# Kernel optimization log

Hardware: AMD Instinct MI355X
Metric: run time of the kernel (lower is better)

Reference implementation:

```python
import jax, jax.numpy as jnp
import numpy as np

E = 1024
H = 16
DH = E // H
EPS = 1e-8
GRAM_W = 1.5


def _gram_scores(q, k1, k2):
    # q: [BH, L, D], k1/k2: [BH, S, D] -> [BH, L, S]
    ll = jnp.sum(q * q, -1)[:, :, None]          # [BH, L, 1]
    vv = jnp.sum(k1 * k1, -1)[:, None, :]        # [BH, 1, S]
    aa = jnp.sum(k2 * k2, -1)[:, None, :]
    va = jnp.sum(k1 * k2, -1)[:, None, :]
    lv = jnp.einsum('bld,bsd->bls', q, k1)
    la = jnp.einsum('bld,bsd->bls', q, k2)
    det = ll * (vv * aa - va * va) - lv * (lv * aa - la * va) + la * (lv * va - la * vv)
    return -jnp.sqrt(jnp.clip(det, EPS, None))


def setup_inputs() -> dict:
    key = jax.random.key(0)
    ks = jax.random.split(key, 20)
    L, B, S = 512, 4, 1024
    inp = {
        'query': jax.random.normal(ks[0], (L, B, E), jnp.float32),
        'mod1': jax.random.normal(ks[1], (S, B, E), jnp.float32),
        'mod2': jax.random.normal(ks[2], (S, B, E), jnp.float32),
    }
    # Linear params stored as [in, out] (y = x @ W + b), 8 linears
    names = ['q', 'k1', 'k2', 'v1', 'v2', 'g1', 'g2', 'o']
    for i, n in enumerate(names):
        inp[n + '_w'] = jax.random.normal(ks[3 + 2 * i], (E, E), jnp.float32) * 0.02
        inp[n + '_b'] = jax.random.normal(ks[4 + 2 * i], (E,), jnp.float32) * 0.02
    return inp


def reference(query, mod1, mod2,
              q_w, q_b, k1_w, k1_b, k2_w, k2_b, v1_w, v1_b, v2_w, v2_b,
              g1_w, g1_b, g2_w, g2_b, o_w, o_b):
    L, B, _ = query.shape
    S = mod1.shape[0]
    scaling = DH ** -0.5

    def lin(x, w, b):
        return x @ w + b

    def split_heads(x, n):  # [n, B, E] -> [B*H, n, DH]
        return x.reshape(n, B * H, DH).transpose(1, 0, 2)

    q = split_heads(lin(query, q_w, q_b) * scaling, L)
    k1 = split_heads(lin(mod1, k1_w, k1_b), S)
    k2 = split_heads(lin(mod2, k2_w, k2_b), S)
    v1 = split_heads(lin(mod1, v1_w, v1_b), S)
    v2 = split_heads(lin(mod2, v2_w, v2_b), S)

    w1 = jnp.einsum('bld,bsd->bls', q, k1)
    w2 = jnp.einsum('bld,bsd->bls', q, k2)
    gram = _gram_scores(q, k1, k2)
    logits = GRAM_W * gram + w1 + w2          # [BH, L, S]
    attn = jax.nn.softmax(logits, axis=-1)

    def merge_heads(x):  # [B*H, L, DH] -> [L, B, E]
        return x.transpose(1, 0, 2).reshape(L, B, E)

    out1 = merge_heads(jnp.einsum('bls,bsd->bld', attn, v1))
    out2 = merge_heads(jnp.einsum('bls,bsd->bld', attn, v2))
    gate1 = jax.nn.sigmoid(lin(query, g1_w, g1_b))
    gate2 = jax.nn.sigmoid(lin(query, g2_w, g2_b))
    attn_output = lin((out1 * gate1 + out2 * gate2) / 2.0, o_w, o_b)
    avg_weights = attn.reshape(B, H, L, S).mean(axis=1)
    return attn_output, avg_weights
```

## Files before the change

kernel.cpp:

```cpp
#include <hip/hip_runtime.h>
#include <cstddef>
#include <cstdint>

typedef unsigned short ushort_t;
typedef unsigned int uint_t;
typedef __attribute__((ext_vector_type(8))) short short8;
typedef __attribute__((ext_vector_type(4))) float f32x4;

#define EDIM 1024
#define NHEAD 16
#define HDIM 64
#define NB 4
#define LQ 512
#define SK 1024
#define BHD 64

__device__ __forceinline__ ushort_t f2b(float f) {
    uint_t u = __float_as_uint(f);
    return (ushort_t)((u + 0x7fffu + ((u >> 16) & 1u)) >> 16);
}
__device__ __forceinline__ float b2f(ushort_t b) {
    return __uint_as_float(((uint_t)b) << 16);
}

__device__ __forceinline__ void gload_lds16(const void* g, void* l) {
    __builtin_amdgcn_global_load_lds((const __attribute__((address_space(1))) void*)g,
                                     (__attribute__((address_space(3))) void*)l, 16, 0, 0);
}

template<int OUTMODE>
__global__ __launch_bounds__(256, 2)
void gemm_mfma(const ushort_t* __restrict__ Ah, const ushort_t* __restrict__ Al,
               const ushort_t* __restrict__ Bh, const ushort_t* __restrict__ Bl,
               const float* __restrict__ b0, const float* __restrict__ b1,
               const float* __restrict__ b2,
               void* __restrict__ Y0, void* __restrict__ Y1, void* __restrict__ Y2,
               float scale)
{
    __shared__ ushort_t As[128 * 64];
    __shared__ ushort_t Bs[128 * 64];
    const int tid = threadIdx.x;
    const int wave = tid >> 6, lane = tid & 63;
    const int ln = lane & 15, lq = lane >> 4;
    const int row0 = blockIdx.y * 128, col0 = blockIdx.x * 128;
    const int wm = wave & 1, wn = wave >> 1;
    const int cswz = (lane & 7) ^ ((lane >> 3) & 7);
    const int mrl = lane >> 3;

    const int seg = (OUTMODE == 0) ? 0 : (blockIdx.x >> 3);
    const int NPASS = (OUTMODE == 5 && seg == 0) ? 3 : 1;

    f32x4 zero = {0.f, 0.f, 0.f, 0.f};
    f32x4 acc[4][4];
#pragma unroll
    for (int i = 0; i < 4; ++i)
#pragma unroll
        for (int j = 0; j < 4; ++j) acc[i][j] = zero;

    for (int pp = 0; pp < NPASS; ++pp) {
        const ushort_t* Ab = (pp == 2) ? Al : Ah;
        const ushort_t* Bb = (pp == 1) ? Bl : Bh;
        for (int kk = 0; kk < 1024; kk += 64) {
            __syncthreads();
#pragma unroll
            for (int j = 0; j < 4; ++j) {
                const int mr = (wave * 4 + j) * 8 + mrl;
                gload_lds16(Ab + (size_t)(row0 + mr) * 1024 + kk + cswz * 8,
                            (void*)(As + (wave * 4 + j) * 512));
                gload_lds16(Bb + (size_t)(col0 + mr) * 1024 + kk + cswz * 8,
                            (void*)(Bs + (wave * 4 + j) * 512));
            }
            __syncthreads();
#pragma unroll
            for (int sub = 0; sub < 2; ++sub) {
                short8 af[4], bfv[4];
#pragma unroll
                for (int i = 0; i < 4; ++i) {
                    const int ml = wm * 64 + i * 16 + ln;
                    af[i] = *(const short8*)(As + ml * 64 + (((sub * 4 + lq) ^ (ml & 7)) * 8));
                    const int nl = wn * 64 + i * 16 + ln;
                    bfv[i] = *(const short8*)(Bs + nl * 64 + (((sub * 4 + lq) ^ (nl & 7)) * 8));
                }
#pragma unroll
                for (int i = 0; i < 4; ++i)
#pragma unroll
                    for (int j = 0; j < 4; ++j)
                        acc[i][j] = __builtin_amdgcn_mfma_f32_16x16x32_bf16(af[i], bfv[j], acc[i][j], 0, 0, 0);
            }
        }
    }

    const float* bias = (seg == 0) ? b0 : ((seg == 1) ? b1 : b2);

#pragma unroll
    for (int i = 0; i < 4; ++i) {
#pragma unroll
        for (int r = 0; r < 4; ++r) {
            const int row = row0 + wm * 64 + i * 16 + lq * 4 + r;
#pragma unroll
            for (int j = 0; j < 4; ++j) {
                const int col = col0 + wn * 64 + j * 16 + ln;
                const int lc = col & 1023;
                float v = acc[i][j][r] + bias[lc];
                if (OUTMODE == 0) {
                    ((float*)Y0)[(size_t)row * 1024 + lc] = v;
                } else if (OUTMODE == 4) {
                    if (seg == 0) {
                        v *= scale;
                        const int s = row >> 2, b = row & 3, h = lc >> 6, d = lc & 63;
                        ((ushort_t*)Y0)[(((size_t)(b * 16 + h)) * 512 + s) * 64 + d] = f2b(v);
                    } else {
                        v = 1.0f / (1.0f + __expf(-v));
                        float* Y = (seg == 1) ? (float*)Y1 : (float*)Y2;
                        Y[(size_t)row * 1024 + lc] = v;
                    }
                } else {
                    const int s = row >> 2, b = row & 3, h = lc >> 6, d = lc & 63;
                    const size_t addr = (((size_t)(b * 16 + h)) * 1024 + s) * 64 + d;
                    if (seg == 0) ((float*)Y0)[addr] = v;
                    else          ((ushort_t*)Y1)[addr] = f2b(v);
                }
            }
        }
    }
}

__global__ __launch_bounds__(256)
void cast_q_kernel(const float* __restrict__ x, ushort_t* __restrict__ y)
{
    const size_t i = ((size_t)blockIdx.x * 256 + threadIdx.x) * 8;
    float4 a = *(const float4*)(x + i);
    float4 b = *(const float4*)(x + i + 4);
    ushort_t o[8] = {f2b(a.x), f2b(a.y), f2b(a.z), f2b(a.w), f2b(b.x), f2b(b.y), f2b(b.z), f2b(b.w)};
    *(uint4*)( (void*)(y + i) ) = *(const uint4*)o;
}

__global__ __launch_bounds__(256)
void cast_mod_kernel(const float* __restrict__ m1, const float* __restrict__ m2,
                     ushort_t* __restrict__ h1, ushort_t* __restrict__ l1,
                     ushort_t* __restrict__ h2, ushort_t* __restrict__ l2)
{
    const float* x = blockIdx.y ? m2 : m1;
    ushort_t* yh = blockIdx.y ? h2 : h1;
    ushort_t* yl = blockIdx.y ? l2 : l1;
    const size_t i = ((size_t)blockIdx.x * 256 + threadIdx.x) * 8;
    float v[8];
    *(float4*)v = *(const float4*)(x + i);
    *(float4*)(v + 4) = *(const float4*)(x + i + 4);
    ushort_t oh[8], ol[8];
#pragma unroll
    for (int k = 0; k < 8; ++k) {
        oh[k] = f2b(v[k]);
        ol[k] = f2b(v[k] - b2f(oh[k]));
    }
    *(uint4*)( (void*)(yh + i) ) = *(const uint4*)oh;
    *(uint4*)( (void*)(yl + i) ) = *(const uint4*)ol;
}

struct WArgs {
    const float* src[8];
    ushort_t* hi[8];
    ushort_t* lo[8];
};
__global__ __launch_bounds__(256)
void wcast_kernel(WArgs args)
{
    __shared__ float T[64][65];
    const int z = blockIdx.z;
    const float* W = args.src[z];
    ushort_t* Th = args.hi[z];
    ushort_t* Tl = args.lo[z];
    const int k0 = blockIdx.x * 64, n0 = blockIdx.y * 64;
    const int tid = threadIdx.x;
    const int r = tid >> 2, cg = (tid & 3) * 16;
#pragma unroll
    for (int u = 0; u < 4; ++u) {
        float4 v = *(const float4*)(W + (size_t)(k0 + r) * 1024 + n0 + cg + u * 4);
        T[r][cg + u * 4 + 0] = v.x; T[r][cg + u * 4 + 1] = v.y;
        T[r][cg + u * 4 + 2] = v.z; T[r][cg + u * 4 + 3] = v.w;
    }
    __syncthreads();
    ushort_t oh[16], ol[16];
#pragma unroll
    for (int u = 0; u < 16; ++u) {
        float v = T[cg + u][r];
        oh[u] = f2b(v);
        ol[u] = f2b(v - b2f(oh[u]));
    }
    ushort_t* dh = Th + (size_t)(n0 + r) * 1024 + k0 + cg;
    *(uint4*)( (void*)dh ) = *(const uint4*)oh;
    *(uint4*)( (void*)(dh + 8) ) = *(const uint4*)(oh + 8);
    if (Tl) {
        ushort_t* dl = Tl + (size_t)(n0 + r) * 1024 + k0 + cg;
        *(uint4*)( (void*)dl ) = *(const uint4*)ol;
        *(uint4*)( (void*)(dl + 8) ) = *(const uint4*)(ol + 8);
    }
}

__global__ __launch_bounds__(256)
void norms_cast_k_kernel(const float* __restrict__ K1f, const float* __restrict__ K2f,
                         ushort_t* __restrict__ K1b, ushort_t* __restrict__ K2b,
                         float* __restrict__ vv, float* __restrict__ aa, float* __restrict__ va)
{
    const int wave = threadIdx.x >> 6, lane = threadIdx.x & 63;
    const int row = blockIdx.x * 4 + wave;
    const float x1 = K1f[(size_t)row * 64 + lane];
    const float x2 = K2f[(size_t)row * 64 + lane];
    K1b[(size_t)row * 64 + lane] = f2b(x1);
    K2b[(size_t)row * 64 + lane] = f2b(x2);
    float s1 = x1 * x1, s2 = x2 * x2, s3 = x1 * x2;
#pragma unroll
    for (int o = 1; o < 64; o <<= 1) {
        s1 += __shfl_xor(s1, o);
        s2 += __shfl_xor(s2, o);
        s3 += __shfl_xor(s3, o);
    }
    if (lane == 0) { vv[row] = s1; aa[row] = s2; va[row] = s3; }
}

__global__ __launch_bounds__(256)
void normsq_kernel(const ushort_t* __restrict__ Qb, float* __restrict__ ll)
{
    const int wave = threadIdx.x >> 6, lane = threadIdx.x & 63;
    const int row = blockIdx.x * 4 + wave;
    const float x = b2f(Qb[(size_t)row * 64 + lane]);
    float s = x * x;
#pragma unroll
    for (int o = 1; o < 64; o <<= 1) s += __shfl_xor(s, o);
    if (lane == 0) ll[row] = s;
}

__global__ __launch_bounds__(256)
void vtrans_kernel(const ushort_t* __restrict__ V1b, const ushort_t* __restrict__ V2b,
                   ushort_t* __restrict__ V1t, ushort_t* __restrict__ V2t)
{
    __shared__ float T[64][65];
    const ushort_t* S = blockIdx.z ? V2b : V1b;
    ushort_t* D = blockIdx.z ? V2t : V1t;
    const int bh = blockIdx.y, s0 = blockIdx.x * 64;
    const int tid = threadIdx.x;
    const int r = tid >> 2, cg = (tid & 3) * 16;
    ushort_t buf[16];
    const ushort_t* sp = S + ((size_t)bh * 1024 + s0 + r) * 64 + cg;
    *(uint4*)buf = *(const uint4*)sp;
    *(uint4*)(buf + 8) = *(const uint4*)(sp + 8);
#pragma unroll
    for (int u = 0; u < 16; ++u) T[r][cg + u] = b2f(buf[u]);
    __syncthreads();
    ushort_t o[16];
#pragma unroll
    for (int u = 0; u < 16; ++u) o[u] = f2b(T[cg + u][r]);
    ushort_t* d = D + ((size_t)bh * 64 + r) * 1024 + s0 + cg;
    *(uint4*)( (void*)d ) = *(const uint4*)o;
    *(uint4*)( (void*)(d + 8) ) = *(const uint4*)(o + 8);
}

__global__ __launch_bounds__(256, 2)
void scores_kernel(const ushort_t* __restrict__ Qb, const ushort_t* __restrict__ K1b,
                   const ushort_t* __restrict__ K2b, const float* __restrict__ ll,
                   const float* __restrict__ vv, const float* __restrict__ aa,
                   const float* __restrict__ va, float* __restrict__ logits)
{
    __shared__ ushort_t Qs[128 * 64];
    __shared__ ushort_t K1s[128 * 64];
    __shared__ ushort_t K2s[128 * 64];
    __shared__ float llS[128], vvS[128], aaS[128], vaS[128];
    const int tid = threadIdx.x;
    const int wave = tid >> 6, lane = tid & 63;
    const int ln = lane & 15, lq = lane >> 4;
    const int wm = wave & 1, wn = wave >> 1;
    const int bh = blockIdx.z;
    const int l0 = blockIdx.y * 128, s0 = blockIdx.x * 128;
    const int cswz = (lane & 7) ^ ((lane >> 3) & 7);
    const int mrl = lane >> 3;

    if (tid < 128) {
        llS[tid] = ll[(size_t)bh * 512 + l0 + tid];
        vvS[tid] = vv[(size_t)bh * 1024 + s0 + tid];
        aaS[tid] = aa[(size_t)bh * 1024 + s0 + tid];
        vaS[tid] = va[(size_t)bh * 1024 + s0 + tid];
    }
#pragma unroll
    for (int j = 0; j < 4; ++j) {
        const int mr = (wave * 4 + j) * 8 + mrl;
        gload_lds16(Qb + ((size_t)bh * 512 + l0 + mr) * 64 + cswz * 8, (void*)(Qs + (wave * 4 + j) * 512));
        gload_lds16(K1b + ((size_t)bh * 1024 + s0 + mr) * 64 + cswz * 8, (void*)(K1s + (wave * 4 + j) * 512));
        gload_lds16(K2b + ((size_t)bh * 1024 + s0 + mr) * 64 + cswz * 8, (void*)(K2s + (wave * 4 + j) * 512));
    }
    __syncthreads();

    f32x4 zero = {0.f, 0.f, 0.f, 0.f};
    f32x4 lv[4][4], la[4][4];
#pragma unroll
    for (int i = 0; i < 4; ++i)
#pragma unroll
        for (int j = 0; j < 4; ++j) { lv[i][j] = zero; la[i][j] = zero; }

#pragma unroll
    for (int sub = 0; sub < 2; ++sub) {
        short8 qf[4], k1f[4], k2f[4];
#pragma unroll
        for (int i = 0; i < 4; ++i) {
            const int ml = wm * 64 + i * 16 + ln;
            qf[i] = *(const short8*)(Qs + ml * 64 + (((sub * 4 + lq) ^ (ml & 7)) * 8));
            const int nl = wn * 64 + i * 16 + ln;
            k1f[i] = *(const short8*)(K1s + nl * 64 + (((sub * 4 + lq) ^ (nl & 7)) * 8));
            k2f[i] = *(const short8*)(K2s + nl * 64 + (((sub * 4 + lq) ^ (nl & 7)) * 8));
        }
#pragma unroll
        for (int i = 0; i < 4; ++i)
#pragma unroll
            for (int j = 0; j < 4; ++j) {
                lv[i][j] = __builtin_amdgcn_mfma_f32_16x16x32_bf16(qf[i], k1f[j], lv[i][j], 0, 0, 0);
                la[i][j] = __builtin_amdgcn_mfma_f32_16x16x32_bf16(qf[i], k2f[j], la[i][j], 0, 0, 0);
            }
    }

#pragma unroll
    for (int i = 0; i < 4; ++i) {
#pragma unroll
        for (int r = 0; r < 4; ++r) {
            const int l_loc = wm * 64 + i * 16 + lq * 4 + r;
            const float LL = llS[l_loc];
#pragma unroll
            for (int j = 0; j < 4; ++j) {
                const int s_loc = wn * 64 + j * 16 + ln;
                const float VV = vvS[s_loc], AA = aaS[s_loc], VA = vaS[s_loc];
                const float LV = lv[i][j][r], LA = la[i][j][r];
                float det = LL * (VV * AA - VA * VA) - LV * (LV * AA - LA * VA) + LA * (LV * VA - LA * VV);
                det = fmaxf(det, 1e-8f);
                logits[((size_t)bh * 512 + l0 + l_loc) * 1024 + s0 + s_loc] = LV + LA - 1.5f * sqrtf(det);
            }
        }
    }
}

__global__ __launch_bounds__(256)
void softmax_avg_kernel(float* __restrict__ logits, float* __restrict__ avg)
{
    __shared__ float part[4][1024];
    const int b = blockIdx.x >> 9, l = blockIdx.x & 511;
    const int wave = threadIdx.x >> 6, lane = threadIdx.x & 63;
    float pacc[16];
#pragma unroll
    for (int u = 0; u < 16; ++u) pacc[u] = 0.f;
#pragma unroll
    for (int jj = 0; jj < 4; ++jj) {
        const int h = wave * 4 + jj;
        float* rowp = logits + (((size_t)(b * 16 + h)) * 512 + l) * 1024;
        float4 v[4];
#pragma unroll
        for (int c = 0; c < 4; ++c) v[c] = *(const float4*)(rowp + c * 256 + lane * 4);
        float m = -3.4e38f;
#pragma unroll
        for (int c = 0; c < 4; ++c) m = fmaxf(m, fmaxf(fmaxf(v[c].x, v[c].y), fmaxf(v[c].z, v[c].w)));
#pragma unroll
        for (int o = 1; o < 64; o <<= 1) m = fmaxf(m, __shfl_xor(m, o));
        float s = 0.f;
#pragma unroll
        for (int c = 0; c < 4; ++c) {
            v[c].x = __expf(v[c].x - m); v[c].y = __expf(v[c].y - m);
            v[c].z = __expf(v[c].z - m); v[c].w = __expf(v[c].w - m);
            s += v[c].x + v[c].y + v[c].z + v[c].w;
        }
#pragma unroll
        for (int o = 1; o < 64; o <<= 1) s += __shfl_xor(s, o);
        const float inv = 1.0f / s;
        ushort_t* arow = (ushort_t*)rowp;
#pragma unroll
        for (int c = 0; c < 4; ++c) {
            const float p0 = v[c].x * inv, p1 = v[c].y * inv, p2 = v[c].z * inv, p3 = v[c].w * inv;
            ushort_t w[4] = {f2b(p0), f2b(p1), f2b(p2), f2b(p3)};
            *(uint2*)( (void*)(arow + c * 256 + lane * 4) ) = *(const uint2*)w;
            pacc[c * 4 + 0] += p0; pacc[c * 4 + 1] += p1;
            pacc[c * 4 + 2] += p2; pacc[c * 4 + 3] += p3;
        }
    }
#pragma unroll
    for (int c = 0; c < 4; ++c) {
        float4 pv = {pacc[c * 4 + 0], pacc[c * 4 + 1], pacc[c * 4 + 2], pacc[c * 4 + 3]};
        *(float4*)(&part[wave][c * 256 + lane * 4]) = pv;
    }
    __syncthreads();
    const int s0 = threadIdx.x * 4;
    float4 a0 = *(const float4*)(&part[0][s0]);
    float4 a1 = *(const float4*)(&part[1][s0]);
    float4 a2 = *(const float4*)(&part[2][s0]);
    float4 a3 = *(const float4*)(&part[3][s0]);
    float4 o;
    o.x = (a0.x + a1.x + a2.x + a3.x) * 0.0625f;
    o.y = (a0.y + a1.y + a2.y + a3.y) * 0.0625f;
    o.z = (a0.z + a1.z + a2.z + a3.z) * 0.0625f;
    o.w = (a0.w + a1.w + a2.w + a3.w) * 0.0625f;
    *(float4*)(avg + ((size_t)(b * 512 + l)) * 1024 + s0) = o;
}

__global__ __launch_bounds__(256, 2)
void pv_gate_kernel(const ushort_t* __restrict__ attn, const ushort_t* __restrict__ V1t,
                    const ushort_t* __restrict__ V2t, const float* __restrict__ G1,
                    const float* __restrict__ G2, ushort_t* __restrict__ tmpb)
{
    __shared__ ushort_t Ps[128 * 64];
    __shared__ ushort_t V1s[64 * 64];
    __shared__ ushort_t V2s[64 * 64];
    const int tid = threadIdx.x;
    const int wave = tid >> 6, lane = tid & 63;
    const int ln = lane & 15, lq = lane >> 4;
    const int bh = blockIdx.y;
    const int l0 = blockIdx.x * 128;
    const int cswz = (lane & 7) ^ ((lane >> 3) & 7);
    const int mrl = lane >> 3;
    const int bq = bh >> 4, h = bh & 15;

    f32x4 zero = {0.f, 0.f, 0.f, 0.f};
    f32x4 acc1[2][4], acc2[2][4];
#pragma unroll
    for (int i = 0; i < 2; ++i)
#pragma unroll
        for (int j = 0; j < 4; ++j) { acc1[i][j] = zero; acc2[i][j] = zero; }

    for (int s0 = 0; s0 < 1024; s0 += 64) {
        __syncthreads();
#pragma unroll
        for (int j = 0; j < 4; ++j) {
            const int mr = (wave * 4 + j) * 8 + mrl;
            gload_lds16(attn + ((size_t)bh * 512 + l0 + mr) * 2048 + s0 + cswz * 8,
                        (void*)(Ps + (wave * 4 + j) * 512));
        }
#pragma unroll
        for (int j = 0; j < 2; ++j) {
            const int mv = (wave * 2 + j) * 8 + mrl;
            gload_lds16(V1t + ((size_t)bh * 64 + mv) * 1024 + s0 + cswz * 8,
                        (void*)(V1s + (wave * 2 + j) * 512));
            gload_lds16(V2t + ((size_t)bh * 64 + mv) * 1024 + s0 + cswz * 8,
                        (void*)(V2s + (wave * 2 + j) * 512));
        }
        __syncthreads();
#pragma unroll
        for (int sub = 0; sub < 2; ++sub) {
            short8 af[2], b1f[4], b2f_[4];
#pragma unroll
            for (int i = 0; i < 2; ++i) {
                const int ml = wave * 32 + i * 16 + ln;
                af[i] = *(const short8*)(Ps + ml * 64 + (((sub * 4 + lq) ^ (ml & 7)) * 8));
            }
#pragma unroll
            for (int j = 0; j < 4; ++j) {
                const int nl = j * 16 + ln;
                b1f[j] = *(const short8*)(V1s + nl * 64 + (((sub * 4 + lq) ^ (nl & 7)) * 8));
                b2f_[j] = *(const short8*)(V2s + nl * 64 + (((sub * 4 + lq) ^ (nl & 7)) * 8));
            }
#pragma unroll
            for (int i = 0; i < 2; ++i)
#pragma unroll
                for (int j = 0; j < 4; ++j) {
                    acc1[i][j] = __builtin_amdgcn_mfma_f32_16x16x32_bf16(af[i], b1f[j], acc1[i][j], 0, 0, 0);
                    acc2[i][j] = __builtin_amdgcn_mfma_f32_16x16x32_bf16(af[i], b2f_[j], acc2[i][j], 0, 0, 0);
                }
        }
    }

#pragma unroll
    for (int i = 0; i < 2; ++i) {
#pragma unroll
        for (int r = 0; r < 4; ++r) {
            const int l = l0 + wave * 32 + i * 16 + lq * 4 + r;
#pragma unroll
            for (int j = 0; j < 4; ++j) {
                const int d = j * 16 + ln;
                const size_t addr = ((size_t)l * 4 + bq) * 1024 + h * 64 + d;
                const float v = 0.5f * (acc1[i][j][r] * G1[addr] + acc2[i][j][r] * G2[addr]);
                tmpb[addr] = f2b(v);
            }
        }
    }
}

extern "C" void kernel_launch(void* const* d_in, const int* in_sizes, int n_in,
                              void* d_out, int out_size, void* d_ws, size_t ws_size,
                              hipStream_t stream)
{
    const float* query = (const float*)d_in[0];
    const float* mod1  = (const float*)d_in[1];
    const float* mod2  = (const float*)d_in[2];
    const float* q_w  = (const float*)d_in[3];  const float* q_b  = (const float*)d_in[4];
    const float* k1_w = (const float*)d_in[5];  const float* k1_b = (const float*)d_in[6];
    const float* k2_w = (const float*)d_in[7];  const float* k2_b = (const float*)d_in[8];
    const float* v1_w = (const float*)d_in[9];  const float* v1_b = (const float*)d_in[10];
    const float* v2_w = (const float*)d_in[11]; const float* v2_b = (const float*)d_in[12];
    const float* g1_w = (const float*)d_in[13]; const float* g1_b = (const float*)d_in[14];
    const float* g2_w = (const float*)d_in[15]; const float* g2_b = (const float*)d_in[16];
    const float* o_w  = (const float*)d_in[17]; const float* o_b  = (const float*)d_in[18];
    float* out = (float*)d_out;

    const size_t MB = 1u << 20;
    char* w = (char*)d_ws;
    ushort_t* Wqg  = (ushort_t*)(w + 0 * MB);
    ushort_t* Wkv1 = (ushort_t*)(w + 6 * MB);
    ushort_t* Wkv2 = (ushort_t*)(w + 10 * MB);
    ushort_t* Wo   = (ushort_t*)(w + 14 * MB);
    ushort_t* Wk1l = (ushort_t*)(w + 16 * MB);
    ushort_t* Wk2l = (ushort_t*)(w + 18 * MB);
    ushort_t* qx   = (ushort_t*)(w + 20 * MB);
    ushort_t* tmpb = qx;
    ushort_t* m1h  = (ushort_t*)(w + 24 * MB);
    ushort_t* m2h  = (ushort_t*)(w + 32 * MB);
    float* G1 = (float*)(w + 24 * MB);
    float* G2 = (float*)(w + 32 * MB);
    ushort_t* Qb  = (ushort_t*)(w + 40 * MB);
    ushort_t* K1b = (ushort_t*)(w + 44 * MB);
    ushort_t* K2b = (ushort_t*)(w + 52 * MB);
    ushort_t* V1t = (ushort_t*)(w + 60 * MB);
    ushort_t* V2t = (ushort_t*)(w + 68 * MB);
    float* ll = (float*)(w + 76 * MB);
    float* vv = (float*)(w + 76 * MB + 256 * 1024);
    float* aa = (float*)(w + 76 * MB + 512 * 1024);
    float* va = (float*)(w + 76 * MB + 768 * 1024);
    float* logits = (float*)(w + 78 * MB);
    float* K1f = (float*)(w + 78 * MB);
    float* K2f = (float*)(w + 94 * MB);
    ushort_t* V1b = (ushort_t*)(w + 110 * MB);
    ushort_t* V2b = (ushort_t*)(w + 118 * MB);
    ushort_t* m1l = (ushort_t*)(w + 190 * MB);
    ushort_t* m2l = (ushort_t*)(w + 198 * MB);
    ushort_t* attn = (ushort_t*)logits;

    cast_q_kernel<<<1024, 256, 0, stream>>>(query, qx);
    cast_mod_kernel<<<dim3(2048, 2), 256, 0, stream>>>(mod1, mod2, m1h, m1l, m2h, m2l);
    WArgs wa;
    const float* srcs[8] = {q_w, g1_w, g2_w, k1_w, v1_w, k2_w, v2_w, o_w};
    ushort_t* his[8] = {Wqg, Wqg + (size_t)1024 * 1024, Wqg + (size_t)2048 * 1024,
                        Wkv1, Wkv1 + (size_t)1024 * 1024, Wkv2, Wkv2 + (size_t)1024 * 1024, Wo};
    ushort_t* los[8] = {nullptr, nullptr, nullptr, Wk1l, nullptr, Wk2l, nullptr, nullptr};
    for (int i = 0; i < 8; ++i) { wa.src[i] = srcs[i]; wa.hi[i] = his[i]; wa.lo[i] = los[i]; }
    wcast_kernel<<<dim3(16, 16, 8), 256, 0, stream>>>(wa);

    gemm_mfma<5><<<dim3(16, 32), 256, 0, stream>>>(m1h, m1l, Wkv1, Wk1l, k1_b, v1_b, nullptr,
                                                   K1f, V1b, nullptr, 1.f);
    gemm_mfma<5><<<dim3(16, 32), 256, 0, stream>>>(m2h, m2l, Wkv2, Wk2l, k2_b, v2_b, nullptr,
                                                   K2f, V2b, nullptr, 1.f);
    gemm_mfma<4><<<dim3(24, 16), 256, 0, stream>>>(qx, nullptr, Wqg, nullptr, q_b, g1_b, g2_b,
                                                   Qb, G1, G2, 0.125f);

    norms_cast_k_kernel<<<16384, 256, 0, stream>>>(K1f, K2f, K1b, K2b, vv, aa, va);
    normsq_kernel<<<8192, 256, 0, stream>>>(Qb, ll);
    vtrans_kernel<<<dim3(16, 64, 2), 256, 0, stream>>>(V1b, V2b, V1t, V2t);

    scores_kernel<<<dim3(8, 4, 64), 256, 0, stream>>>(Qb, K1b, K2b, ll, vv, aa, va, logits);
    softmax_avg_kernel<<<2048, 256, 0, stream>>>(logits, out + (size_t)LQ * NB * EDIM);
    pv_gate_kernel<<<dim3(4, 64), 256, 0, stream>>>(attn, V1t, V2t, G1, G2, tmpb);

    gemm_mfma<0><<<dim3(8, 16), 256, 0, stream>>>(tmpb, nullptr, Wo, nullptr, o_b, nullptr, nullptr,
                                                  out, nullptr, nullptr, 1.f);
}
```

Baseline: 436.1 us.

## Merge projection GEMMs, cast and prep kernels into fewer launches

Combines the three cast kernels into one launch and the three input-projection GEMMs into a single grid. In that grid the 3-pass split-precision K blocks are separated from the 1-pass V blocks, so per-block work is more uniform. The norm, norm-squared and V-transpose kernels are merged into one prep launch, gates are stored as bf16 instead of fp32, and the output projection uses 64-row tiles to put more blocks on the device. The intent is to cut launch gaps and tail effects and to reduce gate memory traffic, at the cost of bf16 rounding on the gate values.

```diff
diff --git a/kernel.cpp b/kernel.cpp
--- a/kernel.cpp
+++ b/kernel.cpp
@@ -28,27 +28,51 @@
                                      (__attribute__((address_space(3))) void*)l, 16, 0, 0);
 }
 
-template<int OUTMODE>
+struct MegaArgs {
+    const ushort_t *qx, *m1h, *m1l, *m2h, *m2l;
+    const ushort_t *Wqg, *Wkv1, *Wkv2, *Wk1l, *Wk2l;
+    const float *q_b, *k1_b, *k2_b, *v1_b, *v2_b, *g1_b, *g2_b;
+    float *K1f, *K2f;
+    ushort_t *V1b, *V2b, *Qb, *G1b, *G2b;
+};
+
 __global__ __launch_bounds__(256, 2)
-void gemm_mfma(const ushort_t* __restrict__ Ah, const ushort_t* __restrict__ Al,
-               const ushort_t* __restrict__ Bh, const ushort_t* __restrict__ Bl,
-               const float* __restrict__ b0, const float* __restrict__ b1,
-               const float* __restrict__ b2,
-               void* __restrict__ Y0, void* __restrict__ Y1, void* __restrict__ Y2,
-               float scale)
+void mega_gemm(MegaArgs a)
 {
     __shared__ ushort_t As[128 * 64];
     __shared__ ushort_t Bs[128 * 64];
     const int tid = threadIdx.x;
     const int wave = tid >> 6, lane = tid & 63;
     const int ln = lane & 15, lq = lane >> 4;
-    const int row0 = blockIdx.y * 128, col0 = blockIdx.x * 128;
     const int wm = wave & 1, wn = wave >> 1;
     const int cswz = (lane & 7) ^ ((lane >> 3) & 7);
     const int mrl = lane >> 3;
 
-    const int seg = (OUTMODE == 0) ? 0 : (blockIdx.x >> 3);
-    const int NPASS = (OUTMODE == 5 && seg == 0) ? 3 : 1;
+    const int id = blockIdx.x;
+    const ushort_t *A, *Al, *B, *Bl;
+    const float* bias;
+    int npass, row0, col0, kind;
+    if (id < 512) {
+        kind = id >> 8;
+        const int t = id & 255;
+        col0 = (t & 7) * 128; row0 = (t >> 3) * 128; npass = 3;
+        A = kind ? a.m2h : a.m1h;  Al = kind ? a.m2l : a.m1l;
+        B = kind ? a.Wkv2 : a.Wkv1; Bl = kind ? a.Wk2l : a.Wk1l;
+        bias = kind ? a.k2_b : a.k1_b;
+    } else if (id < 1024) {
+        int t = id - 512; kind = 2 + (t >> 8); t &= 255;
+        col0 = (t & 7) * 128; row0 = (t >> 3) * 128; npass = 1;
+        A = (kind == 2) ? a.m1h : a.m2h; Al = A;
+        B = ((kind == 2) ? a.Wkv1 : a.Wkv2) + (size_t)1024 * 1024; Bl = B;
+        bias = (kind == 2) ? a.v1_b : a.v2_b;
+    } else {
+        const int t = id - 1024; kind = 4;
+        const int c = t % 24, rr = t / 24;
+        col0 = c * 128; row0 = rr * 128; npass = 1;
+        A = a.qx; Al = A; B = a.Wqg; Bl = B;
+        const int seg = c >> 3;
+        bias = (seg == 0) ? a.q_b : ((seg == 1) ? a.g1_b : a.g2_b);
+    }
 
     f32x4 zero = {0.f, 0.f, 0.f, 0.f};
     f32x4 acc[4][4];
@@ -57,9 +81,9 @@
 #pragma unroll
         for (int j = 0; j < 4; ++j) acc[i][j] = zero;
 
-    for (int pp = 0; pp < NPASS; ++pp) {
-        const ushort_t* Ab = (pp == 2) ? Al : Ah;
-        const ushort_t* Bb = (pp == 1) ? Bl : Bh;
+    for (int pp = 0; pp < npass; ++pp) {
+        const ushort_t* Ab = (pp == 2) ? Al : A;
+        const ushort_t* Bb = (pp == 1) ? Bl : B;
         for (int kk = 0; kk < 1024; kk += 64) {
             __syncthreads();
 #pragma unroll
@@ -90,8 +114,6 @@
         }
     }
 
-    const float* bias = (seg == 0) ? b0 : ((seg == 1) ? b1 : b2);
-
 #pragma unroll
     for (int i = 0; i < 4; ++i) {
 #pragma unroll
@@ -102,157 +124,155 @@
                 const int col = col0 + wn * 64 + j * 16 + ln;
                 const int lc = col & 1023;
                 float v = acc[i][j][r] + bias[lc];
-                if (OUTMODE == 0) {
-                    ((float*)Y0)[(size_t)row * 1024 + lc] = v;
-                } else if (OUTMODE == 4) {
+                if (kind <= 1) {
+                    const int s = row >> 2, b = row & 3, h = lc >> 6, d = lc & 63;
+                    float* Y = kind ? a.K2f : a.K1f;
+                    Y[(((size_t)(b * 16 + h)) * 1024 + s) * 64 + d] = v;
+                } else if (kind <= 3) {
+                    const int s = row >> 2, b = row & 3, h = lc >> 6, d = lc & 63;
+                    ushort_t* Y = (kind == 2) ? a.V1b : a.V2b;
+                    Y[(((size_t)(b * 16 + h)) * 1024 + s) * 64 + d] = f2b(v);
+                } else {
+                    const int seg = col >> 10;
                     if (seg == 0) {
-                        v *= scale;
+                        v *= 0.125f;
                         const int s = row >> 2, b = row & 3, h = lc >> 6, d = lc & 63;
-                        ((ushort_t*)Y0)[(((size_t)(b * 16 + h)) * 512 + s) * 64 + d] = f2b(v);
+                        a.Qb[(((size_t)(b * 16 + h)) * 512 + s) * 64 + d] = f2b(v);
                     } else {
                         v = 1.0f / (1.0f + __expf(-v));
-                        float* Y = (seg == 1) ? (float*)Y1 : (float*)Y2;
-                        Y[(size_t)row * 1024 + lc] = v;
+                        ushort_t* Y = (seg == 1) ? a.G1b : a.G2b;
+                        Y[(size_t)row * 1024 + lc] = f2b(v);
                     }
-                } else {
-                    const int s = row >> 2, b = row & 3, h = lc >> 6, d = lc & 63;
-                    const size_t addr = (((size_t)(b * 16 + h)) * 1024 + s) * 64 + d;
-                    if (seg == 0) ((float*)Y0)[addr] = v;
-                    else          ((ushort_t*)Y1)[addr] = f2b(v);
                 }
             }
         }
     }
 }
 
+struct CastArgs {
+    const float* q; const float* m1; const float* m2;
+    ushort_t* qx; ushort_t* m1h; ushort_t* m1l; ushort_t* m2h; ushort_t* m2l;
+    const float* wsrc[8];
+    ushort_t* whi[8];
+    ushort_t* wlo[8];
+};
+
 __global__ __launch_bounds__(256)
-void cast_q_kernel(const float* __restrict__ x, ushort_t* __restrict__ y)
-{
-    const size_t i = ((size_t)blockIdx.x * 256 + threadIdx.x) * 8;
-    float4 a = *(const float4*)(x + i);
-    float4 b = *(const float4*)(x + i + 4);
-    ushort_t o[8] = {f2b(a.x), f2b(a.y), f2b(a.z), f2b(a.w), f2b(b.x), f2b(b.y), f2b(b.z), f2b(b.w)};
-    *(uint4*)( (void*)(y + i) ) = *(const uint4*)o;
+void casts_kernel(CastArgs a)
+{
+    __shared__ float T[64][65];
+    const int id = blockIdx.x;
+    const int tid = threadIdx.x;
+    if (id < 1024) {
+        const size_t i = ((size_t)id * 256 + tid) * 8;
+        float4 x = *(const float4*)(a.q + i);
+        float4 y = *(const float4*)(a.q + i + 4);
+        ushort_t o[8] = {f2b(x.x), f2b(x.y), f2b(x.z), f2b(x.w), f2b(y.x), f2b(y.y), f2b(y.z), f2b(y.w)};
+        *(uint4*)( (void*)(a.qx + i) ) = *(const uint4*)o;
+    } else if (id < 5120) {
+        const int t = id - 1024;
+        const int which = t >> 11;
+        const float* x = which ? a.m2 : a.m1;
+        ushort_t* yh = which ? a.m2h : a.m1h;
+        ushort_t* yl = which ? a.m2l : a.m1l;
+        const size_t i = ((size_t)(t & 2047) * 256 + tid) * 8;
+        float v[8];
+        *(float4*)v = *(const float4*)(x + i);
+        *(float4*)(v + 4) = *(const float4*)(x + i + 4);
+        ushort_t oh[8], ol[8];
+#pragma unroll
+        for (int k = 0; k < 8; ++k) {
+            oh[k] = f2b(v[k]);
+            ol[k] = f2b(v[k] - b2f(oh[k]));
+        }
+        *(uint4*)( (void*)(yh + i) ) = *(const uint4*)oh;
+        *(uint4*)( (void*)(yl + i) ) = *(const uint4*)ol;
+    } else {
+        const int t = id - 5120;
+        const int z = t >> 8, x = t & 15, y = (t >> 4) & 15;
+        const float* W = a.wsrc[z];
+        ushort_t* Th = a.whi[z];
+        ushort_t* Tl = a.wlo[z];
+        const int k0 = x * 64, n0 = y * 64;
+        const int r = tid >> 2, cg = (tid & 3) * 16;
+#pragma unroll
+        for (int u = 0; u < 4; ++u) {
+            float4 v = *(const float4*)(W + (size_t)(k0 + r) * 1024 + n0 + cg + u * 4);
+            T[r][cg + u * 4 + 0] = v.x; T[r][cg + u * 4 + 1] = v.y;
+            T[r][cg + u * 4 + 2] = v.z; T[r][cg + u * 4 + 3] = v.w;
+        }
+        __syncthreads();
+        ushort_t oh[16], ol[16];
+#pragma unroll
+        for (int u = 0; u < 16; ++u) {
+            float v = T[cg + u][r];
+            oh[u] = f2b(v);
+            ol[u] = f2b(v - b2f(oh[u]));
+        }
+        ushort_t* dh = Th + (size_t)(n0 + r) * 1024 + k0 + cg;
+        *(uint4*)( (void*)dh ) = *(const uint4*)oh;
+        *(uint4*)( (void*)(dh + 8) ) = *(const uint4*)(oh + 8);
+        if (Tl) {
+            ushort_t* dl = Tl + (size_t)(n0 + r) * 1024 + k0 + cg;
+            *(uint4*)( (void*)dl ) = *(const uint4*)ol;
+            *(uint4*)( (void*)(dl + 8) ) = *(const uint4*)(ol + 8);
+        }
+    }
 }
 
 __global__ __launch_bounds__(256)
-void cast_mod_kernel(const float* __restrict__ m1, const float* __restrict__ m2,
-                     ushort_t* __restrict__ h1, ushort_t* __restrict__ l1,
-                     ushort_t* __restrict__ h2, ushort_t* __restrict__ l2)
-{
-    const float* x = blockIdx.y ? m2 : m1;
-    ushort_t* yh = blockIdx.y ? h2 : h1;
-    ushort_t* yl = blockIdx.y ? l2 : l1;
-    const size_t i = ((size_t)blockIdx.x * 256 + threadIdx.x) * 8;
-    float v[8];
-    *(float4*)v = *(const float4*)(x + i);
-    *(float4*)(v + 4) = *(const float4*)(x + i + 4);
-    ushort_t oh[8], ol[8];
-#pragma unroll
-    for (int k = 0; k < 8; ++k) {
-        oh[k] = f2b(v[k]);
-        ol[k] = f2b(v[k] - b2f(oh[k]));
-    }
-    *(uint4*)( (void*)(yh + i) ) = *(const uint4*)oh;
-    *(uint4*)( (void*)(yl + i) ) = *(const uint4*)ol;
-}
-
-struct WArgs {
-    const float* src[8];
-    ushort_t* hi[8];
-    ushort_t* lo[8];
-};
-__global__ __launch_bounds__(256)
-void wcast_kernel(WArgs args)
+void prep_kernel(const float* __restrict__ K1f, const float* __restrict__ K2f,
+                 ushort_t* __restrict__ K1b, ushort_t* __restrict__ K2b,
+                 float* __restrict__ vv, float* __restrict__ aa, float* __restrict__ va,
+                 const ushort_t* __restrict__ Qb, float* __restrict__ ll,
+                 const ushort_t* __restrict__ V1b, const ushort_t* __restrict__ V2b,
+                 ushort_t* __restrict__ V1t, ushort_t* __restrict__ V2t)
 {
     __shared__ float T[64][65];
-    const int z = blockIdx.z;
-    const float* W = args.src[z];
-    ushort_t* Th = args.hi[z];
-    ushort_t* Tl = args.lo[z];
-    const int k0 = blockIdx.x * 64, n0 = blockIdx.y * 64;
+    const int id = blockIdx.x;
     const int tid = threadIdx.x;
-    const int r = tid >> 2, cg = (tid & 3) * 16;
-#pragma unroll
-    for (int u = 0; u < 4; ++u) {
-        float4 v = *(const float4*)(W + (size_t)(k0 + r) * 1024 + n0 + cg + u * 4);
-        T[r][cg + u * 4 + 0] = v.x; T[r][cg + u * 4 + 1] = v.y;
-        T[r][cg + u * 4 + 2] = v.z; T[r][cg + u * 4 + 3] = v.w;
-    }
-    __syncthreads();
-    ushort_t oh[16], ol[16];
-#pragma unroll
-    for (int u = 0; u < 16; ++u) {
-        float v = T[cg + u][r];
-        oh[u] = f2b(v);
-        ol[u] = f2b(v - b2f(oh[u]));
-    }
-    ushort_t* dh = Th + (size_t)(n0 + r) * 1024 + k0 + cg;
-    *(uint4*)( (void*)dh ) = *(const uint4*)oh;
-    *(uint4*)( (void*)(dh + 8) ) = *(const uint4*)(oh + 8);
-    if (Tl) {
-        ushort_t* dl = Tl + (size_t)(n0 + r) * 1024 + k0 + cg;
-        *(uint4*)( (void*)dl ) = *(const uint4*)ol;
-        *(uint4*)( (void*)(dl + 8) ) = *(const uint4*)(ol + 8);
-    }
-}
-
-__global__ __launch_bounds__(256)
-void norms_cast_k_kernel(const float* __restrict__ K1f, const float* __restrict__ K2f,
-                         ushort_t* __restrict__ K1b, ushort_t* __restrict__ K2b,
-                         float* __restrict__ vv, float* __restrict__ aa, float* __restrict__ va)
-{
-    const int wave = threadIdx.x >> 6, lane = threadIdx.x & 63;
-    const int row = blockIdx.x * 4 + wave;
-    const float x1 = K1f[(size_t)row * 64 + lane];
-    const float x2 = K2f[(size_t)row * 64 + lane];
-    K1b[(size_t)row * 64 + lane] = f2b(x1);
-    K2b[(size_t)row * 64 + lane] = f2b(x2);
-    float s1 = x1 * x1, s2 = x2 * x2, s3 = x1 * x2;
-#pragma unroll
-    for (int o = 1; o < 64; o <<= 1) {
-        s1 += __shfl_xor(s1, o);
-        s2 += __shfl_xor(s2, o);
-        s3 += __shfl_xor(s3, o);
-    }
-    if (lane == 0) { vv[row] = s1; aa[row] = s2; va[row] = s3; }
-}
-
-__global__ __launch_bounds__(256)
-void normsq_kernel(const ushort_t* __restrict__ Qb, float* __restrict__ ll)
-{
-    const int wave = threadIdx.x >> 6, lane = threadIdx.x & 63;
-    const int row = blockIdx.x * 4 + wave;
-    const float x = b2f(Qb[(size_t)row * 64 + lane]);
-    float s = x * x;
-#pragma unroll
-    for (int o = 1; o < 64; o <<= 1) s += __shfl_xor(s, o);
-    if (lane == 0) ll[row] = s;
-}
-
-__global__ __launch_bounds__(256)
-void vtrans_kernel(const ushort_t* __restrict__ V1b, const ushort_t* __restrict__ V2b,
-                   ushort_t* __restrict__ V1t, ushort_t* __restrict__ V2t)
-{
-    __shared__ float T[64][65];
-    const ushort_t* S = blockIdx.z ? V2b : V1b;
-    ushort_t* D = blockIdx.z ? V2t : V1t;
-    const int bh = blockIdx.y, s0 = blockIdx.x * 64;
-    const int tid = threadIdx.x;
-    const int r = tid >> 2, cg = (tid & 3) * 16;
-    ushort_t buf[16];
-    const ushort_t* sp = S + ((size_t)bh * 1024 + s0 + r) * 64 + cg;
-    *(uint4*)buf = *(const uint4*)sp;
-    *(uint4*)(buf + 8) = *(const uint4*)(sp + 8);
-#pragma unroll
-    for (int u = 0; u < 16; ++u) T[r][cg + u] = b2f(buf[u]);
-    __syncthreads();
-    ushort_t o[16];
-#pragma unroll
-    for (int u = 0; u < 16; ++u) o[u] = f2b(T[cg + u][r]);
-    ushort_t* d = D + ((size_t)bh * 64 + r) * 1024 + s0 + cg;
-    *(uint4*)( (void*)d ) = *(const uint4*)o;
-    *(uint4*)( (void*)(d + 8) ) = *(const uint4*)(o + 8);
+    const int wave = tid >> 6, lane = tid & 63;
+    if (id < 16384) {
+        const int row = id * 4 + wave;
+        const float x1 = K1f[(size_t)row * 64 + lane];
+        const float x2 = K2f[(size_t)row * 64 + lane];
+        K1b[(size_t)row * 64 + lane] = f2b(x1);
+        K2b[(size_t)row * 64 + lane] = f2b(x2);
+        float s1 = x1 * x1, s2 = x2 * x2, s3 = x1 * x2;
+#pragma unroll
+        for (int o = 1; o < 64; o <<= 1) {
+            s1 += __shfl_xor(s1, o);
+            s2 += __shfl_xor(s2, o);
+            s3 += __shfl_xor(s3, o);
+        }
+        if (lane == 0) { vv[row] = s1; aa[row] = s2; va[row] = s3; }
+    } else if (id < 24576) {
+        const int row = (id - 16384) * 4 + wave;
+        const float x = b2f(Qb[(size_t)row * 64 + lane]);
+        float s = x * x;
+#pragma unroll
+        for (int o = 1; o < 64; o <<= 1) s += __shfl_xor(s, o);
+        if (lane == 0) ll[row] = s;
+    } else {
+        const int t = id - 24576;
+        const int z = t >> 10, bh = (t >> 4) & 63, s0 = (t & 15) * 64;
+        const ushort_t* S = z ? V2b : V1b;
+        ushort_t* D = z ? V2t : V1t;
+        const int r = tid >> 2, cg = (tid & 3) * 16;
+        ushort_t buf[16];
+        const ushort_t* sp = S + ((size_t)bh * 1024 + s0 + r) * 64 + cg;
+        *(uint4*)buf = *(const uint4*)sp;
+        *(uint4*)(buf + 8) = *(const uint4*)(sp + 8);
+#pragma unroll
+        for (int u = 0; u < 16; ++u) T[r][cg + u] = b2f(buf[u]);
+        __syncthreads();
+        ushort_t o[16];
+#pragma unroll
+        for (int u = 0; u < 16; ++u) o[u] = f2b(T[cg + u][r]);
+        ushort_t* d = D + ((size_t)bh * 64 + r) * 1024 + s0 + cg;
+        *(uint4*)( (void*)d ) = *(const uint4*)o;
+        *(uint4*)( (void*)(d + 8) ) = *(const uint4*)(o + 8);
+    }
 }
 
 __global__ __launch_bounds__(256, 2)
@@ -397,8 +417,8 @@
 
 __global__ __launch_bounds__(256, 2)
 void pv_gate_kernel(const ushort_t* __restrict__ attn, const ushort_t* __restrict__ V1t,
-                    const ushort_t* __restrict__ V2t, const float* __restrict__ G1,
-                    const float* __restrict__ G2, ushort_t* __restrict__ tmpb)
+                    const ushort_t* __restrict__ V2t, const ushort_t* __restrict__ G1,
+                    const ushort_t* __restrict__ G2, ushort_t* __restrict__ tmpb)
 {
     __shared__ ushort_t Ps[128 * 64];
     __shared__ ushort_t V1s[64 * 64];
@@ -469,8 +489,79 @@
             for (int j = 0; j < 4; ++j) {
                 const int d = j * 16 + ln;
                 const size_t addr = ((size_t)l * 4 + bq) * 1024 + h * 64 + d;
-                const float v = 0.5f * (acc1[i][j][r] * G1[addr] + acc2[i][j][r] * G2[addr]);
+                const float v = 0.5f * (acc1[i][j][r] * b2f(G1[addr]) + acc2[i][j][r] * b2f(G2[addr]));
                 tmpb[addr] = f2b(v);
+            }
+        }
+    }
+}
+
+__global__ __launch_bounds__(256, 2)
+void gemm_o64(const ushort_t* __restrict__ A, const ushort_t* __restrict__ B,
+              const float* __restrict__ bias, float* __restrict__ Y)
+{
+    __shared__ ushort_t As[64 * 64];
+    __shared__ ushort_t Bs[128 * 64];
+    const int tid = threadIdx.x;
+    const int wave = tid >> 6, lane = tid & 63;
+    const int ln = lane & 15, lq = lane >> 4;
+    const int row0 = blockIdx.y * 64, col0 = blockIdx.x * 128;
+    const int wm = wave & 1, wn = wave >> 1;
+    const int cswz = (lane & 7) ^ ((lane >> 3) & 7);
+    const int mrl = lane >> 3;
+
+    f32x4 zero = {0.f, 0.f, 0.f, 0.f};
+    f32x4 acc[2][4];
+#pragma unroll
+    for (int i = 0; i < 2; ++i)
+#pragma unroll
+        for (int j = 0; j < 4; ++j) acc[i][j] = zero;
+
+    for (int kk = 0; kk < 1024; kk += 64) {
+        __syncthreads();
+#pragma unroll
+        for (int j = 0; j < 2; ++j) {
+            const int mr = (wave * 2 + j) * 8 + mrl;
+            gload_lds16(A + (size_t)(row0 + mr) * 1024 + kk + cswz * 8,
+                        (void*)(As + (wave * 2 + j) * 512));
+        }
+#pragma unroll
+        for (int j = 0; j < 4; ++j) {
+            const int mr = (wave * 4 + j) * 8 + mrl;
+            gload_lds16(B + (size_t)(col0 + mr) * 1024 + kk + cswz * 8,
+                        (void*)(Bs + (wave * 4 + j) * 512));
+        }
+        __syncthreads();
+#pragma unroll
+        for (int sub = 0; sub < 2; ++sub) {
+            short8 af[2], bfv[4];
+#pragma unroll
+            for (int i = 0; i < 2; ++i) {
+                const int ml = wm * 32 + i * 16 + ln;
+                af[i] = *(const short8*)(As + ml * 64 + (((sub * 4 + lq) ^ (ml & 7)) * 8));
+            }
+#pragma unroll
+            for (int j = 0; j < 4; ++j) {
+                const int nl = wn * 64 + j * 16 + ln;
+                bfv[j] = *(const short8*)(Bs + nl * 64 + (((sub * 4 + lq) ^ (nl & 7)) * 8));
+            }
+#pragma unroll
+            for (int i = 0; i < 2; ++i)
+#pragma unroll
+                for (int j = 0; j < 4; ++j)
+                    acc[i][j] = __builtin_amdgcn_mfma_f32_16x16x32_bf16(af[i], bfv[j], acc[i][j], 0, 0, 0);
+        }
+    }
+
+#pragma unroll
+    for (int i = 0; i < 2; ++i) {
+#pragma unroll
+        for (int r = 0; r < 4; ++r) {
+            const int row = row0 + wm * 32 + i * 16 + lq * 4 + r;
+#pragma unroll
+            for (int j = 0; j < 4; ++j) {
+                const int col = col0 + wn * 64 + j * 16 + ln;
+                Y[(size_t)row * 1024 + col] = acc[i][j][r] + bias[col];
             }
         }
     }
@@ -503,53 +594,52 @@
     ushort_t* Wk2l = (ushort_t*)(w + 18 * MB);
     ushort_t* qx   = (ushort_t*)(w + 20 * MB);
     ushort_t* tmpb = qx;
-    ushort_t* m1h  = (ushort_t*)(w + 24 * MB);
-    ushort_t* m2h  = (ushort_t*)(w + 32 * MB);
-    float* G1 = (float*)(w + 24 * MB);
-    float* G2 = (float*)(w + 32 * MB);
-    ushort_t* Qb  = (ushort_t*)(w + 40 * MB);
-    ushort_t* K1b = (ushort_t*)(w + 44 * MB);
-    ushort_t* K2b = (ushort_t*)(w + 52 * MB);
-    ushort_t* V1t = (ushort_t*)(w + 60 * MB);
-    ushort_t* V2t = (ushort_t*)(w + 68 * MB);
-    float* ll = (float*)(w + 76 * MB);
-    float* vv = (float*)(w + 76 * MB + 256 * 1024);
-    float* aa = (float*)(w + 76 * MB + 512 * 1024);
-    float* va = (float*)(w + 76 * MB + 768 * 1024);
+    ushort_t* Qb   = (ushort_t*)(w + 24 * MB);
+    ushort_t* K1b  = (ushort_t*)(w + 28 * MB);
+    ushort_t* K2b  = (ushort_t*)(w + 36 * MB);
+    ushort_t* V1t  = (ushort_t*)(w + 44 * MB);
+    ushort_t* V2t  = (ushort_t*)(w + 52 * MB);
+    ushort_t* G1b  = (ushort_t*)(w + 60 * MB);
+    ushort_t* G2b  = (ushort_t*)(w + 64 * MB);
+    float* ll = (float*)(w + 68 * MB);
+    float* vv = (float*)(w + 68 * MB + 256 * 1024);
+    float* aa = (float*)(w + 68 * MB + 512 * 1024);
+    float* va = (float*)(w + 68 * MB + 768 * 1024);
     float* logits = (float*)(w + 78 * MB);
-    float* K1f = (float*)(w + 78 * MB);
-    float* K2f = (float*)(w + 94 * MB);
-    ushort_t* V1b = (ushort_t*)(w + 110 * MB);
-    ushort_t* V2b = (ushort_t*)(w + 118 * MB);
-    ushort_t* m1l = (ushort_t*)(w + 190 * MB);
-    ushort_t* m2l = (ushort_t*)(w + 198 * MB);
+    ushort_t* m1h = (ushort_t*)(w + 78 * MB);
+    ushort_t* m2h = (ushort_t*)(w + 86 * MB);
+    ushort_t* m1l = (ushort_t*)(w + 94 * MB);
+    ushort_t* m2l = (ushort_t*)(w + 102 * MB);
+    float* K1f = (float*)(w + 110 * MB);
+    float* K2f = (float*)(w + 126 * MB);
+    ushort_t* V1b = (ushort_t*)(w + 142 * MB);
+    ushort_t* V2b = (ushort_t*)(w + 150 * MB);
     ushort_t* attn = (ushort_t*)logits;
 
-    cast_q_kernel<<<1024, 256, 0, stream>>>(query, qx);
-    cast_mod_kernel<<<dim3(2048, 2), 256, 0, stream>>>(mod1, mod2, m1h, m1l, m2h, m2l);
-    WArgs wa;
+    CastArgs ca;
+    ca.q = query; ca.m1 = mod1; ca.m2 = mod2;
+    ca.qx = qx; ca.m1h = m1h; ca.m1l = m1l; ca.m2h = m2h; ca.m2l = m2l;
     const float* srcs[8] = {q_w, g1_w, g2_w, k1_w, v1_w, k2_w, v2_w, o_w};
     ushort_t* his[8] = {Wqg, Wqg + (size_t)1024 * 1024, Wqg + (size_t)2048 * 1024,
                         Wkv1, Wkv1 + (size_t)1024 * 1024, Wkv2, Wkv2 + (size_t)1024 * 1024, Wo};
     ushort_t* los[8] = {nullptr, nullptr, nullptr, Wk1l, nullptr, Wk2l, nullptr, nullptr};
-    for (int i = 0; i < 8; ++i) { wa.src[i] = srcs[i]; wa.hi[i] = his[i]; wa.lo[i] = los[i]; }
-    wcast_kernel<<<dim3(16, 16, 8), 256, 0, stream>>>(wa);
-
-    gemm_mfma<5><<<dim3(16, 32), 256, 0, stream>>>(m1h, m1l, Wkv1, Wk1l, k1_b, v1_b, nullptr,
-                                                   K1f, V1b, nullptr, 1.f);
-    gemm_mfma<5><<<dim3(16, 32), 256, 0, stream>>>(m2h, m2l, Wkv2, Wk2l, k2_b, v2_b, nullptr,
-                                                   K2f, V2b, nullptr, 1.f);
-    gemm_mfma<4><<<dim3(24, 16), 256, 0, stream>>>(qx, nullptr, Wqg, nullptr, q_b, g1_b, g2_b,
-                                                   Qb, G1, G2, 0.125f);
-
-    norms_cast_k_kernel<<<16384, 256, 0, stream>>>(K1f, K2f, K1b, K2b, vv, aa, va);
-    normsq_kernel<<<8192, 256, 0, stream>>>(Qb, ll);
-    vtrans_kernel<<<dim3(16, 64, 2), 256, 0, stream>>>(V1b, V2b, V1t, V2t);
+    for (int i = 0; i < 8; ++i) { ca.wsrc[i] = srcs[i]; ca.whi[i] = his[i]; ca.wlo[i] = los[i]; }
+    casts_kernel<<<7168, 256, 0, stream>>>(ca);
+
+    MegaArgs ma;
+    ma.qx = qx; ma.m1h = m1h; ma.m1l = m1l; ma.m2h = m2h; ma.m2l = m2l;
+    ma.Wqg = Wqg; ma.Wkv1 = Wkv1; ma.Wkv2 = Wkv2; ma.Wk1l = Wk1l; ma.Wk2l = Wk2l;
+    ma.q_b = q_b; ma.k1_b = k1_b; ma.k2_b = k2_b; ma.v1_b = v1_b; ma.v2_b = v2_b;
+    ma.g1_b = g1_b; ma.g2_b = g2_b;
+    ma.K1f = K1f; ma.K2f = K2f; ma.V1b = V1b; ma.V2b = V2b;
+    ma.Qb = Qb; ma.G1b = G1b; ma.G2b = G2b;
+    mega_gemm<<<1408, 256, 0, stream>>>(ma);
+
+    prep_kernel<<<26624, 256, 0, stream>>>(K1f, K2f, K1b, K2b, vv, aa, va,
+                                           Qb, ll, V1b, V2b, V1t, V2t);
 
     scores_kernel<<<dim3(8, 4, 64), 256, 0, stream>>>(Qb, K1b, K2b, ll, vv, aa, va, logits);
     softmax_avg_kernel<<<2048, 256, 0, stream>>>(logits, out + (size_t)LQ * NB * EDIM);
-    pv_gate_kernel<<<dim3(4, 64), 256, 0, stream>>>(attn, V1t, V2t, G1, G2, tmpb);
-
-    gemm_mfma<0><<<dim3(8, 16), 256, 0, stream>>>(tmpb, nullptr, Wo, nullptr, o_b, nullptr, nullptr,
-                                                  out, nullptr, nullptr, 1.f);
-}
+    pv_gate_kernel<<<dim3(4, 64), 256, 0, stream>>>(attn, V1t, V2t, G1b, G2b, tmpb);
+    gemm_o64<<<dim3(8, 32), 256, 0, stream>>>(tmpb, Wo, o_b, out);
+}
```

Result: faster. 397.4 us (-8.9%).
